# Kernel tuning notes

Hardware: AMD Instinct MI355X
Metric: run time of the kernel (lower is better)

Reference implementation:

```python
import jax, jax.numpy as jnp
import numpy as np

IN_CH = 64
EMBED = 128
OUT_CH = 64
NUM_HEADS = 2
HEAD_DIM = EMBED // NUM_HEADS
B, D, H, W = 2, 16, 16, 16
SEQ = D * H * W


def setup_inputs() -> dict:
    key = jax.random.key(0)
    ks = jax.random.split(key, 12)
    s = lambda fan_in: 1.0 / np.sqrt(fan_in)
    return {
        "x": jax.random.normal(ks[0], (B, IN_CH, D, H, W), dtype=jnp.float32),
        "W_cp": jax.random.uniform(ks[1], (EMBED, IN_CH), jnp.float32, -s(IN_CH), s(IN_CH)),
        "b_cp": jax.random.uniform(ks[2], (EMBED,), jnp.float32, -s(IN_CH), s(IN_CH)),
        "W_q": jax.random.uniform(ks[3], (EMBED, EMBED), jnp.float32, -s(EMBED), s(EMBED)),
        "W_k": jax.random.uniform(ks[4], (EMBED, EMBED), jnp.float32, -s(EMBED), s(EMBED)),
        "W_v": jax.random.uniform(ks[5], (EMBED, EMBED), jnp.float32, -s(EMBED), s(EMBED)),
        "W_o": jax.random.uniform(ks[6], (EMBED, EMBED), jnp.float32, -s(EMBED), s(EMBED)),
        "b_o": jax.random.uniform(ks[7], (EMBED,), jnp.float32, -s(EMBED), s(EMBED)),
        "W_out": jax.random.uniform(ks[8], (OUT_CH, EMBED), jnp.float32, -s(EMBED), s(EMBED)),
        "b_out": jax.random.uniform(ks[9], (OUT_CH,), jnp.float32, -s(EMBED), s(EMBED)),
        "pos": jax.random.normal(ks[10], (1, SEQ, EMBED), dtype=jnp.float32) * 0.02,
        "gate": jnp.float32(0.1),
    }


def reference(x, W_cp, b_cp, W_q, W_k, W_v, W_o, b_o, W_out, b_out, pos, gate):
    b, c, d, h, w = x.shape
    seq = d * h * w
    scale = HEAD_DIM ** (-0.5)
    # (B, C, D, H, W) -> (B, S, C)
    xf = jnp.transpose(x, (0, 2, 3, 4, 1)).reshape(b, seq, c)
    xf = xf @ W_cp.T + b_cp + pos  # (B, S, E)
    # QKV projections, split heads: (B, nh, S, hd)
    def heads(t):
        return jnp.transpose(t.reshape(b, seq, NUM_HEADS, HEAD_DIM), (0, 2, 1, 3))
    q = heads(xf @ W_q.T)
    k = heads(xf @ W_k.T)
    v = heads(xf @ W_v.T)
    attn = jax.nn.softmax(jnp.einsum("bnsd,bntd->bnst", q, k) * scale, axis=-1)
    o = jnp.einsum("bnst,bntd->bnsd", attn, v)  # (B, nh, S, hd)
    o = jnp.transpose(o, (0, 2, 1, 3)).reshape(b, seq, EMBED)
    o = o @ W_o.T + b_o
    o = o @ W_out.T + b_out  # (B, S, out)
    out = jnp.transpose(o, (0, 2, 1)).reshape(b, OUT_CH, d, h, w)
    # in_channels == output_dim -> skip is identity (no conv/BN in original)
    return out + gate * x
```

## Files before the change

kernel.cpp:

```cpp
#include <hip/hip_runtime.h>
#include <hip/hip_bf16.h>
#include <cstdint>

typedef unsigned short u16;
typedef __attribute__((ext_vector_type(8))) short short8;
typedef __attribute__((ext_vector_type(8))) float f32x8;
typedef __attribute__((ext_vector_type(4))) float f32x4;

#define MFMA(a, b, c) __builtin_amdgcn_mfma_f32_16x16x32_bf16((a), (b), (c), 0, 0, 0)

#define SEQ 4096
#define KSPLIT 8
#define NTILE (SEQ / KSPLIT / 32)

static __device__ __forceinline__ float b2f(u16 u) {
    union { float f; uint32_t i; } c; c.i = ((uint32_t)u) << 16; return c.f;
}
static __device__ __forceinline__ u16 f2b(float f) {
    union { float f; uint32_t i; } c; c.f = f;
    uint32_t r = c.i + 0x7FFF + ((c.i >> 16) & 1);
    return (u16)(r >> 16);
}
static __device__ __forceinline__ short8 ld8(const u16* p) {
    return *reinterpret_cast<const short8*>(p);
}
static __device__ __forceinline__ uint32_t pk2(float a, float b) {
    uint32_t r;
    asm("v_cvt_pk_bf16_f32 %0, %1, %2" : "=v"(r) : "v"(a), "v"(b));
    return r;
}
static __device__ __forceinline__ void gld16(const u16* g, u16* l) {
    __builtin_amdgcn_global_load_lds(
        (const __attribute__((address_space(1))) unsigned int*)g,
        (__attribute__((address_space(3))) unsigned int*)l, 16, 0, 0);
}

__global__ void k_prep(const float* __restrict__ Wo, const float* __restrict__ bo,
                       const float* __restrict__ Wout, const float* __restrict__ bout,
                       const float* __restrict__ Wcp, const float* __restrict__ Wq,
                       const float* __restrict__ Wk, const float* __restrict__ Wv,
                       u16* __restrict__ Wc, float* __restrict__ bc,
                       u16* __restrict__ Wcp_b, u16* __restrict__ Wq_b,
                       u16* __restrict__ Wk_b, u16* __restrict__ Wv_b) {
    int idx = blockIdx.x * 256 + threadIdx.x;
    if (idx < 8192) {
        int co = idx >> 7, e = idx & 127;
        float s = 0.f;
        for (int k = 0; k < 128; k++)
            s += Wout[co * 128 + k] * Wo[k * 128 + e];
        Wc[idx] = f2b(s);
    } else if (idx < 8256) {
        int co = idx - 8192;
        float s = bout[co];
        for (int k = 0; k < 128; k++)
            s += bo[k] * Wout[co * 128 + k];
        bc[co] = s;
    } else if (idx < 16448) {
        int i = idx - 8256;  Wcp_b[i] = f2b(Wcp[i]);
    } else if (idx < 32832) {
        int i = idx - 16448; Wq_b[i] = f2b(Wq[i]);
    } else if (idx < 49216) {
        int i = idx - 32832; Wk_b[i] = f2b(Wk[i]);
    } else if (idx < 65600) {
        int i = idx - 49216; Wv_b[i] = f2b(Wv[i]);
    }
}

__global__ __launch_bounds__(256) void k_front(const float* __restrict__ x,
                                               const u16* __restrict__ Wcp,
                                               const float* __restrict__ bcp,
                                               const float* __restrict__ pos,
                                               const u16* __restrict__ Wq,
                                               const u16* __restrict__ Wk,
                                               const u16* __restrict__ Wv,
                                               u16* __restrict__ Q, u16* __restrict__ K,
                                               u16* __restrict__ V) {
    __shared__ __align__(16) u16 xT[32][72];
    __shared__ __align__(16) u16 xfl[32 * 128];
    int blk = blockIdx.x;
    int b = blk >> 7, sb = (blk & 127) * 32;
    int t = threadIdx.x, w = t >> 6, l = t & 63, lc = l & 15, lg = l >> 4;

    {
        int c = t & 63, so = t >> 6;
        const float* src = x + ((size_t)b * 64 + c) * SEQ + sb + so * 8;
        f32x8 a0 = *reinterpret_cast<const f32x8*>(src);
#pragma unroll
        for (int j = 0; j < 8; j++) xT[so * 8 + j][c] = f2b(a0[j]);
    }
    __syncthreads();

    {
        int rt = w >> 1, eh = w & 1;
        short8 af[2];
        af[0] = ld8(&xT[rt * 16 + lc][lg * 8]);
        af[1] = ld8(&xT[rt * 16 + lc][32 + lg * 8]);
#pragma unroll
        for (int et = 0; et < 4; et++) {
            int nt = eh * 4 + et;
            f32x4 acc = {0.f, 0.f, 0.f, 0.f};
#pragma unroll
            for (int ks = 0; ks < 2; ks++) {
                short8 bfr = ld8(Wcp + (nt * 16 + lc) * 64 + ks * 32 + lg * 8);
                acc = MFMA(af[ks], bfr, acc);
            }
            int e = nt * 16 + lc;
            float be = bcp[e];
            int chunk = e >> 3;
#pragma unroll
            for (int r = 0; r < 4; r++) {
                int sl = rt * 16 + lg * 4 + r;
                float v = acc[r] + be + pos[(size_t)(sb + sl) * 128 + e];
                xfl[sl * 128 + ((chunk ^ (sl & 7)) << 3) + (e & 7)] = f2b(v);
            }
        }
    }
    __syncthreads();

    {
        int st = w & 1, hr = w >> 1;
        short8 afq[4];
#pragma unroll
        for (int ks = 0; ks < 4; ks++)
            afq[ks] = ld8(&xfl[(st * 16 + lc) * 128 + (((ks * 4 + lg) ^ (lc & 7)) << 3)]);

        const float qscl = 0.18033688011112042f;
#pragma unroll
        for (int qk = 0; qk < 2; qk++) {
            const u16* W = qk ? Wk : Wq;
            u16* dst = qk ? K : Q;
#pragma unroll
            for (int et = 0; et < 4; et++) {
                int nt = hr * 4 + et;
                f32x4 acc = {0.f, 0.f, 0.f, 0.f};
#pragma unroll
                for (int ks = 0; ks < 4; ks++) {
                    short8 bfr = ld8(W + (nt * 16 + lc) * 128 + ks * 32 + lg * 8);
                    acc = MFMA(afq[ks], bfr, acc);
                }
                int e = nt * 16 + lc, h = e >> 6, d = e & 63;
                float scl = qk ? 1.0f : qscl;
#pragma unroll
                for (int r = 0; r < 4; r++) {
                    int sr = sb + st * 16 + lg * 4 + r;
                    dst[(((size_t)b * 2 + h) * SEQ + sr) * 64 + d] = f2b(acc[r] * scl);
                }
            }
        }
#pragma unroll
        for (int et = 0; et < 4; et++) {
            int nt = hr * 4 + et;
            f32x4 acc = {0.f, 0.f, 0.f, 0.f};
            short8 wv[4];
#pragma unroll
            for (int ks = 0; ks < 4; ks++)
                wv[ks] = ld8(Wv + (nt * 16 + lc) * 128 + ks * 32 + lg * 8);
#pragma unroll
            for (int ks = 0; ks < 4; ks++)
                acc = MFMA(wv[ks], afq[ks], acc);
#pragma unroll
            for (int r = 0; r < 4; r++) {
                int d = nt * 16 + lg * 4 + r, h = d >> 6, dd = d & 63;
                V[((size_t)(b * 2 + h) * 64 + dd) * SEQ + sb + st * 16 + lc] = f2b(acc[r]);
            }
        }
    }
}

__global__ __launch_bounds__(256, 8) void k_attn(const u16* __restrict__ Q,
                                                 const u16* __restrict__ K,
                                                 const u16* __restrict__ Vg,
                                                 u16* __restrict__ Op,
                                                 float2* __restrict__ ml) {
    __shared__ __align__(16) u16 Klds[2][2048];
    __shared__ __align__(16) u16 Vlds[2][2048];
    __shared__ __align__(16) u16 Pl[4][16][32];
    int blk = blockIdx.x;
    int split = blk >> 8, bh = (blk >> 6) & 3, qb = (blk & 63) * 64;
    int kbase = split * (SEQ / KSPLIT);
    const u16* Qp = Q + (size_t)bh * SEQ * 64;
    const u16* Kp = K + (size_t)bh * SEQ * 64;
    const u16* Vp = Vg + (size_t)bh * SEQ * 64;
    int t = threadIdx.x, w = t >> 6, l = t & 63, lc = l & 15, lg = l >> 4;
    uint32_t* plw = (uint32_t*)&Pl[w][0][0];

    const u16* kSrc = Kp + (size_t)(kbase + w * 8 + (l >> 3)) * 64 + (((l & 7) ^ (l >> 3)) << 3);
    const u16* vSrc = Vp + (size_t)(w * 16 + (l >> 2)) * SEQ + kbase + (((l & 3) ^ ((l >> 3) & 3)) << 3);

    short8 qa[2];
    qa[0] = ld8(Qp + (size_t)(qb + w * 16 + lc) * 64 + lg * 8);
    qa[1] = ld8(Qp + (size_t)(qb + w * 16 + lc) * 64 + 32 + lg * 8);

    short8 onesb;
#pragma unroll
    for (int i = 0; i < 8; i++) onesb[i] = (short)0x3F80;

    f32x4 oacc[4], lsacc = {0.f, 0.f, 0.f, 0.f};
#pragma unroll
    for (int i = 0; i < 4; i++) oacc[i] = (f32x4){0.f, 0.f, 0.f, 0.f};
    float m = -INFINITY;

    int c0 = (lg ^ (lc & 7)) * 8;
    int cv = (lg ^ ((lc >> 1) & 3)) * 8;

#define STAGE(buf, tt) do {                                       \
        gld16(kSrc + (size_t)(tt) * 2048, &Klds[buf][w * 512]);   \
        gld16(vSrc + (tt) * 32,           &Vlds[buf][w * 512]);   \
    } while (0)

    STAGE(0, 0);
    __syncthreads();

#pragma unroll 2
    for (int tt = 0; tt < NTILE; tt++) {
        int cur = tt & 1;
        if (tt + 1 < NTILE) STAGE(cur ^ 1, tt + 1);

        const u16* kb = Klds[cur];
        const u16* vb = Vlds[cur];

        f32x4 sc[2];
#pragma unroll
        for (int nt = 0; nt < 2; nt++) {
            sc[nt] = (f32x4){0.f, 0.f, 0.f, 0.f};
            short8 kf0 = ld8(kb + (nt * 16 + lc) * 64 + c0);
            short8 kf1 = ld8(kb + (nt * 16 + lc) * 64 + (c0 ^ 32));
            sc[nt] = MFMA(kf0, qa[0], sc[nt]);
            sc[nt] = MFMA(kf1, qa[1], sc[nt]);
        }

        float mx = fmaxf(fmaxf(fmaxf(sc[0][0], sc[0][1]), fmaxf(sc[0][2], sc[0][3])),
                         fmaxf(fmaxf(sc[1][0], sc[1][1]), fmaxf(sc[1][2], sc[1][3])));

        if (__any(mx - m > 8.f)) {
            float mr = fmaxf(mx, __shfl_xor(mx, 16));
            mr = fmaxf(mr, __shfl_xor(mr, 32));
            float mn = fmaxf(m, mr);
            float corr = exp2f(m - mn);
#pragma unroll
            for (int r = 0; r < 4; r++) {
                float cr = __shfl(corr, lg * 4 + r);
#pragma unroll
                for (int dt = 0; dt < 4; dt++) oacc[dt][r] *= cr;
                lsacc[r] *= cr;
            }
            m = mn;
        }

        uint32_t pk0 = pk2(exp2f(sc[0][0] - m), exp2f(sc[0][1] - m));
        uint32_t pk1 = pk2(exp2f(sc[0][2] - m), exp2f(sc[0][3] - m));
        uint32_t pk2w = pk2(exp2f(sc[1][0] - m), exp2f(sc[1][1] - m));
        uint32_t pk3 = pk2(exp2f(sc[1][2] - m), exp2f(sc[1][3] - m));

        {
            int rb2 = lc * 16 + (lg & 1) * 2;
            int ph0 = ((lg >> 1) ^ ((lc >> 1) & 3)) * 4;
            int ph1 = ((2 + (lg >> 1)) ^ ((lc >> 1) & 3)) * 4;
            uint2 u0; u0.x = pk0; u0.y = pk1;
            uint2 u1; u1.x = pk2w; u1.y = pk3;
            *reinterpret_cast<uint2*>(&plw[rb2 + ph0]) = u0;
            *reinterpret_cast<uint2*>(&plw[rb2 + ph1]) = u1;
        }

        short8 pa = ld8(&Pl[w][lc][cv]);
        lsacc = MFMA(pa, onesb, lsacc);
#pragma unroll
        for (int dt = 0; dt < 4; dt++) {
            short8 vf = ld8(vb + (dt * 16 + lc) * 32 + cv);
            oacc[dt] = MFMA(pa, vf, oacc[dt]);
        }
        __syncthreads();
    }
#undef STAGE

    size_t rowbase = (size_t)(split * 4 + bh) * SEQ + qb + w * 16;
#pragma unroll
    for (int dt = 0; dt < 4; dt++)
#pragma unroll
        for (int r = 0; r < 4; r++)
            Op[(rowbase + lg * 4 + r) * 64 + dt * 16 + lc] = f2b(oacc[dt][r]);
    float mrow[4];
#pragma unroll
    for (int r = 0; r < 4; r++) mrow[r] = __shfl(m, lg * 4 + r);
    if (lc == 0) {
#pragma unroll
        for (int r = 0; r < 4; r++) {
            float2 v; v.x = mrow[r]; v.y = lsacc[r];
            ml[rowbase + lg * 4 + r] = v;
        }
    }
}

__global__ __launch_bounds__(256) void k_back(const u16* __restrict__ Op,
                                              const float2* __restrict__ ml,
                                              const u16* __restrict__ Wc,
                                              const float* __restrict__ bc,
                                              const float* __restrict__ x,
                                              const float* __restrict__ gate,
                                              float* __restrict__ out) {
    __shared__ __align__(16) u16 Ol[32 * 128];
    int blk = blockIdx.x;
    int b = blk >> 7, sb = (blk & 127) * 32;
    int t = threadIdx.x, w = t >> 6, l = t & 63, lc = l & 15, lg = l >> 4;
    float g = gate[0];

    {
        int sl = t >> 3, ci = t & 7;
        int h = ci >> 2, d0 = (ci & 3) * 16;
        size_t rp0 = ((size_t)(b * 2 + h) << 12) + sb + sl;
        float2 e[KSPLIT];
        float ms = -INFINITY;
#pragma unroll
        for (int k = 0; k < KSPLIT; k++) {
            e[k] = ml[rp0 + (size_t)k * 16384];
            ms = fmaxf(ms, e[k].x);
        }
        float den = 0.f, c[KSPLIT];
#pragma unroll
        for (int k = 0; k < KSPLIT; k++) {
            c[k] = exp2f(e[k].x - ms);
            den += c[k] * e[k].y;
        }
        float inv = 1.0f / den;
#pragma unroll
        for (int half = 0; half < 2; half++) {
            float acc[8];
#pragma unroll
            for (int j = 0; j < 8; j++) acc[j] = 0.f;
#pragma unroll
            for (int k = 0; k < KSPLIT; k++) {
                short8 a = ld8(Op + (rp0 + (size_t)k * 16384) * 64 + d0 + half * 8);
#pragma unroll
                for (int j = 0; j < 8; j++) acc[j] += c[k] * b2f((u16)a[j]);
            }
            short8 ov;
#pragma unroll
            for (int j = 0; j < 8; j++) ov[j] = (short)f2b(acc[j] * inv);
            int chunk = ci * 2 + half;
            *reinterpret_cast<short8*>(&Ol[sl * 128 + ((chunk ^ (sl & 7)) << 3)]) = ov;
        }
    }
    __syncthreads();

    short8 af[4];
#pragma unroll
    for (int ks = 0; ks < 4; ks++)
        af[ks] = ld8(Wc + (w * 16 + lc) * 128 + ks * 32 + lg * 8);

#pragma unroll
    for (int st = 0; st < 2; st++) {
        f32x4 acc = {0.f, 0.f, 0.f, 0.f};
#pragma unroll
        for (int ks = 0; ks < 4; ks++) {
            short8 bfr = ld8(&Ol[(st * 16 + lc) * 128 + (((ks * 4 + lg) ^ (lc & 7)) << 3)]);
            acc = MFMA(af[ks], bfr, acc);
        }
#pragma unroll
        for (int r = 0; r < 4; r++) {
            int co = w * 16 + lg * 4 + r;
            int s = sb + st * 16 + lc;
            size_t idx = ((size_t)b * 64 + co) * SEQ + s;
            out[idx] = acc[r] + bc[co] + g * x[idx];
        }
    }
}

extern "C" void kernel_launch(void* const* d_in, const int* in_sizes, int n_in,
                              void* d_out, int out_size, void* d_ws, size_t ws_size,
                              hipStream_t stream) {
    const float* x    = (const float*)d_in[0];
    const float* Wcp  = (const float*)d_in[1];
    const float* bcp  = (const float*)d_in[2];
    const float* Wq   = (const float*)d_in[3];
    const float* Wk   = (const float*)d_in[4];
    const float* Wv   = (const float*)d_in[5];
    const float* Wo   = (const float*)d_in[6];
    const float* bo   = (const float*)d_in[7];
    const float* Wout = (const float*)d_in[8];
    const float* bout = (const float*)d_in[9];
    const float* pos  = (const float*)d_in[10];
    const float* gate = (const float*)d_in[11];

    char* ws = (char*)d_ws;
    float2* mlp  = (float2*)(ws);
    u16*    Qb   = (u16*)(ws + (2u << 20));
    u16*    Kb   = (u16*)(ws + (4u << 20));
    u16*    Vt   = (u16*)(ws + (6u << 20));
    u16*    Wc   = (u16*)(ws + (10u << 20));
    float*  bc   = (float*)(ws + (10u << 20) + 16384);
    u16*    Wcp_b = (u16*)(ws + (10u << 20) + 32768);
    u16*    Wq_b  = (u16*)(ws + (10u << 20) + 49152);
    u16*    Wk_b  = (u16*)(ws + (10u << 20) + 81920);
    u16*    Wv_b  = (u16*)(ws + (10u << 20) + 114688);
    u16*    Opb  = (u16*)(ws + (10u << 20) + (512u << 10));
    float* out = (float*)d_out;

    hipLaunchKernelGGL(k_prep, dim3(257), dim3(256), 0, stream,
                       Wo, bo, Wout, bout, Wcp, Wq, Wk, Wv,
                       Wc, bc, Wcp_b, Wq_b, Wk_b, Wv_b);
    hipLaunchKernelGGL(k_front, dim3(256), dim3(256), 0, stream,
                       x, Wcp_b, bcp, pos, Wq_b, Wk_b, Wv_b, Qb, Kb, Vt);
    hipLaunchKernelGGL(k_attn, dim3(256 * KSPLIT), dim3(256), 0, stream, Qb, Kb, Vt, Opb, mlp);
    hipLaunchKernelGGL(k_back, dim3(256), dim3(256), 0, stream, Opb, mlp, Wc, bc, x, gate, out);
}
```

Before: 61.82 us.

## Process two 16-row query tiles per wave to reuse K/V fragments

Each wave in the attention kernel now handles 32 query rows instead of 16, so every K and V fragment loaded from LDS feeds two sets of MFMAs. The grid is halved to 1024 blocks and launch bounds are relaxed to 4 blocks per SM to make room for the doubled accumulators. The P staging buffer and the V LDS swizzle are changed to fit the larger tile. This cuts LDS reads and per-tile overhead per query, but raises register use and gives fewer blocks to hide latency.

New measurement: 60.47 us. 1.02x faster.

```diff
diff --git a/kernel.cpp b/kernel.cpp
--- a/kernel.cpp
+++ b/kernel.cpp
@@ -167,41 +167,52 @@
     }
 }
 
-__global__ __launch_bounds__(256, 8) void k_attn(const u16* __restrict__ Q,
+__global__ __launch_bounds__(256, 4) void k_attn(const u16* __restrict__ Q,
                                                  const u16* __restrict__ K,
                                                  const u16* __restrict__ Vg,
                                                  u16* __restrict__ Op,
                                                  float2* __restrict__ ml) {
     __shared__ __align__(16) u16 Klds[2][2048];
     __shared__ __align__(16) u16 Vlds[2][2048];
-    __shared__ __align__(16) u16 Pl[4][16][32];
+    __shared__ __align__(16) u16 Pl[4][32][32];
     int blk = blockIdx.x;
-    int split = blk >> 8, bh = (blk >> 6) & 3, qb = (blk & 63) * 64;
+    int split = blk >> 7, bh = (blk >> 5) & 3, qb = (blk & 31) * 128;
     int kbase = split * (SEQ / KSPLIT);
     const u16* Qp = Q + (size_t)bh * SEQ * 64;
     const u16* Kp = K + (size_t)bh * SEQ * 64;
     const u16* Vp = Vg + (size_t)bh * SEQ * 64;
     int t = threadIdx.x, w = t >> 6, l = t & 63, lc = l & 15, lg = l >> 4;
     uint32_t* plw = (uint32_t*)&Pl[w][0][0];
+    const u16* plu = &Pl[w][0][0];
 
     const u16* kSrc = Kp + (size_t)(kbase + w * 8 + (l >> 3)) * 64 + (((l & 7) ^ (l >> 3)) << 3);
-    const u16* vSrc = Vp + (size_t)(w * 16 + (l >> 2)) * SEQ + kbase + (((l & 3) ^ ((l >> 3) & 3)) << 3);
-
-    short8 qa[2];
-    qa[0] = ld8(Qp + (size_t)(qb + w * 16 + lc) * 64 + lg * 8);
-    qa[1] = ld8(Qp + (size_t)(qb + w * 16 + lc) * 64 + 32 + lg * 8);
+    int vrow = w * 16 + (l >> 2);
+    int vswz = (l & 3) ^ ((((l >> 2) & 3) + (l >> 4)) & 3);
+    const u16* vSrc = Vp + (size_t)vrow * SEQ + kbase + (vswz << 3);
+
+    short8 qa[2][2];
+#pragma unroll
+    for (int ks = 0; ks < 2; ks++)
+#pragma unroll
+        for (int qh = 0; qh < 2; qh++)
+            qa[ks][qh] = ld8(Qp + (size_t)(qb + w * 32 + qh * 16 + lc) * 64 + ks * 32 + lg * 8);
 
     short8 onesb;
 #pragma unroll
     for (int i = 0; i < 8; i++) onesb[i] = (short)0x3F80;
 
-    f32x4 oacc[4], lsacc = {0.f, 0.f, 0.f, 0.f};
-#pragma unroll
-    for (int i = 0; i < 4; i++) oacc[i] = (f32x4){0.f, 0.f, 0.f, 0.f};
-    float m = -INFINITY;
+    f32x4 oacc[2][4], lsacc[2];
+#pragma unroll
+    for (int qh = 0; qh < 2; qh++) {
+        lsacc[qh] = (f32x4){0.f, 0.f, 0.f, 0.f};
+#pragma unroll
+        for (int dt = 0; dt < 4; dt++) oacc[qh][dt] = (f32x4){0.f, 0.f, 0.f, 0.f};
+    }
+    float m[2] = {-INFINITY, -INFINITY};
 
     int c0 = (lg ^ (lc & 7)) * 8;
-    int cv = (lg ^ ((lc >> 1) & 3)) * 8;
+    int sp = (((lc & 3) + (lc >> 2)) & 3);
+    int cv = (lg ^ sp) * 8;
 
 #define STAGE(buf, tt) do {                                       \
         gld16(kSrc + (size_t)(tt) * 2048, &Klds[buf][w * 512]);   \
@@ -219,75 +230,93 @@
         const u16* kb = Klds[cur];
         const u16* vb = Vlds[cur];
 
-        f32x4 sc[2];
+        f32x4 sc[2][2];
 #pragma unroll
         for (int nt = 0; nt < 2; nt++) {
-            sc[nt] = (f32x4){0.f, 0.f, 0.f, 0.f};
             short8 kf0 = ld8(kb + (nt * 16 + lc) * 64 + c0);
             short8 kf1 = ld8(kb + (nt * 16 + lc) * 64 + (c0 ^ 32));
-            sc[nt] = MFMA(kf0, qa[0], sc[nt]);
-            sc[nt] = MFMA(kf1, qa[1], sc[nt]);
-        }
-
-        float mx = fmaxf(fmaxf(fmaxf(sc[0][0], sc[0][1]), fmaxf(sc[0][2], sc[0][3])),
-                         fmaxf(fmaxf(sc[1][0], sc[1][1]), fmaxf(sc[1][2], sc[1][3])));
-
-        if (__any(mx - m > 8.f)) {
-            float mr = fmaxf(mx, __shfl_xor(mx, 16));
-            mr = fmaxf(mr, __shfl_xor(mr, 32));
-            float mn = fmaxf(m, mr);
-            float corr = exp2f(m - mn);
-#pragma unroll
-            for (int r = 0; r < 4; r++) {
-                float cr = __shfl(corr, lg * 4 + r);
-#pragma unroll
-                for (int dt = 0; dt < 4; dt++) oacc[dt][r] *= cr;
-                lsacc[r] *= cr;
-            }
-            m = mn;
-        }
-
-        uint32_t pk0 = pk2(exp2f(sc[0][0] - m), exp2f(sc[0][1] - m));
-        uint32_t pk1 = pk2(exp2f(sc[0][2] - m), exp2f(sc[0][3] - m));
-        uint32_t pk2w = pk2(exp2f(sc[1][0] - m), exp2f(sc[1][1] - m));
-        uint32_t pk3 = pk2(exp2f(sc[1][2] - m), exp2f(sc[1][3] - m));
-
-        {
-            int rb2 = lc * 16 + (lg & 1) * 2;
-            int ph0 = ((lg >> 1) ^ ((lc >> 1) & 3)) * 4;
-            int ph1 = ((2 + (lg >> 1)) ^ ((lc >> 1) & 3)) * 4;
-            uint2 u0; u0.x = pk0; u0.y = pk1;
-            uint2 u1; u1.x = pk2w; u1.y = pk3;
-            *reinterpret_cast<uint2*>(&plw[rb2 + ph0]) = u0;
-            *reinterpret_cast<uint2*>(&plw[rb2 + ph1]) = u1;
-        }
-
-        short8 pa = ld8(&Pl[w][lc][cv]);
-        lsacc = MFMA(pa, onesb, lsacc);
+#pragma unroll
+            for (int qh = 0; qh < 2; qh++) {
+                f32x4 a = {0.f, 0.f, 0.f, 0.f};
+                a = MFMA(kf0, qa[0][qh], a);
+                a = MFMA(kf1, qa[1][qh], a);
+                sc[nt][qh] = a;
+            }
+        }
+
+        float mx[2];
+#pragma unroll
+        for (int qh = 0; qh < 2; qh++)
+            mx[qh] = fmaxf(
+                fmaxf(fmaxf(sc[0][qh][0], sc[0][qh][1]), fmaxf(sc[0][qh][2], sc[0][qh][3])),
+                fmaxf(fmaxf(sc[1][qh][0], sc[1][qh][1]), fmaxf(sc[1][qh][2], sc[1][qh][3])));
+
+        if (__any((mx[0] - m[0] > 8.f) || (mx[1] - m[1] > 8.f))) {
+#pragma unroll
+            for (int qh = 0; qh < 2; qh++) {
+                float mr = fmaxf(mx[qh], __shfl_xor(mx[qh], 16));
+                mr = fmaxf(mr, __shfl_xor(mr, 32));
+                float mn = fmaxf(m[qh], mr);
+                float corr = exp2f(m[qh] - mn);
+#pragma unroll
+                for (int r = 0; r < 4; r++) {
+                    float cr = __shfl(corr, lg * 4 + r);
+#pragma unroll
+                    for (int dt = 0; dt < 4; dt++) oacc[qh][dt][r] *= cr;
+                    lsacc[qh][r] *= cr;
+                }
+                m[qh] = mn;
+            }
+        }
+
+#pragma unroll
+        for (int qh = 0; qh < 2; qh++) {
+            int rowb = (qh * 16 + lc) * 16 + (lg & 1) * 2;
+#pragma unroll
+            for (int nt = 0; nt < 2; nt++) {
+                uint2 u;
+                u.x = pk2(exp2f(sc[nt][qh][0] - m[qh]), exp2f(sc[nt][qh][1] - m[qh]));
+                u.y = pk2(exp2f(sc[nt][qh][2] - m[qh]), exp2f(sc[nt][qh][3] - m[qh]));
+                int cc = (nt * 2 + (lg >> 1)) ^ sp;
+                *reinterpret_cast<uint2*>(&plw[rowb + cc * 4]) = u;
+            }
+        }
+
+        short8 pa0 = ld8(plu + (lc) * 32 + cv);
+        short8 pa1 = ld8(plu + (16 + lc) * 32 + cv);
+        lsacc[0] = MFMA(pa0, onesb, lsacc[0]);
+        lsacc[1] = MFMA(pa1, onesb, lsacc[1]);
 #pragma unroll
         for (int dt = 0; dt < 4; dt++) {
             short8 vf = ld8(vb + (dt * 16 + lc) * 32 + cv);
-            oacc[dt] = MFMA(pa, vf, oacc[dt]);
+            oacc[0][dt] = MFMA(pa0, vf, oacc[0][dt]);
+            oacc[1][dt] = MFMA(pa1, vf, oacc[1][dt]);
         }
         __syncthreads();
     }
 #undef STAGE
 
-    size_t rowbase = (size_t)(split * 4 + bh) * SEQ + qb + w * 16;
-#pragma unroll
-    for (int dt = 0; dt < 4; dt++)
-#pragma unroll
-        for (int r = 0; r < 4; r++)
-            Op[(rowbase + lg * 4 + r) * 64 + dt * 16 + lc] = f2b(oacc[dt][r]);
-    float mrow[4];
-#pragma unroll
-    for (int r = 0; r < 4; r++) mrow[r] = __shfl(m, lg * 4 + r);
+    size_t rowbase = (size_t)(split * 4 + bh) * SEQ + qb + w * 32;
+#pragma unroll
+    for (int qh = 0; qh < 2; qh++)
+#pragma unroll
+        for (int dt = 0; dt < 4; dt++)
+#pragma unroll
+            for (int r = 0; r < 4; r++)
+                Op[(rowbase + qh * 16 + lg * 4 + r) * 64 + dt * 16 + lc] = f2b(oacc[qh][dt][r]);
+    float mr[2][4];
+#pragma unroll
+    for (int qh = 0; qh < 2; qh++)
+#pragma unroll
+        for (int r = 0; r < 4; r++) mr[qh][r] = __shfl(m[qh], lg * 4 + r);
     if (lc == 0) {
 #pragma unroll
-        for (int r = 0; r < 4; r++) {
-            float2 v; v.x = mrow[r]; v.y = lsacc[r];
-            ml[rowbase + lg * 4 + r] = v;
-        }
+        for (int qh = 0; qh < 2; qh++)
+#pragma unroll
+            for (int r = 0; r < 4; r++) {
+                float2 v; v.x = mr[qh][r]; v.y = lsacc[qh][r];
+                ml[rowbase + qh * 16 + lg * 4 + r] = v;
+            }
     }
 }
 
@@ -400,6 +429,6 @@
                        Wc, bc, Wcp_b, Wq_b, Wk_b, Wv_b);
     hipLaunchKernelGGL(k_front, dim3(256), dim3(256), 0, stream,
                        x, Wcp_b, bcp, pos, Wq_b, Wk_b, Wv_b, Qb, Kb, Vt);
-    hipLaunchKernelGGL(k_attn, dim3(256 * KSPLIT), dim3(256), 0, stream, Qb, Kb, Vt, Opb, mlp);
+    hipLaunchKernelGGL(k_attn, dim3(1024), dim3(256), 0, stream, Qb, Kb, Vt, Opb, mlp);
     hipLaunchKernelGGL(k_back, dim3(256), dim3(256), 0, stream, Opb, mlp, Wc, bc, x, gate, out);
 }
```
